# Performance work log

Hardware: AMD Instinct MI355X
Metric: run time of the kernel (lower is better)

## Reference

```python
import jax, jax.numpy as jnp
import numpy as np
from jax import lax

V, E, H, K = 100000, 256, 512, 12
B, T = 64, 256
START, END, PAD = 10, 11, 0
NEG = -100000.0


def setup_inputs() -> dict:
    key = jax.random.key(0)
    ks = jax.random.split(key, 16)
    Hd = H // 2
    def n(k, shape, s=0.1):
        return jax.random.normal(k, shape, jnp.float32) * s
    sentence = jax.random.randint(ks[0], (B, T), 0, V)
    sentence_chars = jnp.zeros((B, T, 16), jnp.int32)
    emb = jax.random.normal(ks[1], (V, E), jnp.float32)
    Wih_f, Whh_f = n(ks[2], (4 * Hd, E)), n(ks[3], (4 * Hd, Hd))
    bih_f, bhh_f = n(ks[4], (4 * Hd,)), n(ks[5], (4 * Hd,))
    Wih_b, Whh_b = n(ks[6], (4 * Hd, E)), n(ks[7], (4 * Hd, Hd))
    bih_b, bhh_b = n(ks[8], (4 * Hd,)), n(ks[9], (4 * Hd,))
    Wp, bp = n(ks[10], (K, H)), n(ks[11], (K,))
    # transitions[i, j] = score of transitioning from tag j to tag i
    trans = jax.random.normal(ks[12], (K, K), jnp.float32)
    trans = trans.at[START, :].set(NEG)
    trans = trans.at[:, END].set(NEG)
    trans = trans.at[:, PAD].set(NEG)
    trans = trans.at[PAD, :].set(NEG)
    trans = trans.at[PAD, PAD].set(0.0)
    trans = trans.at[PAD, END].set(0.0)
    h0 = jax.random.normal(ks[13], (2, B, Hd), jnp.float32)
    c0 = jax.random.normal(ks[14], (2, B, Hd), jnp.float32)
    return dict(sentence=sentence, sentence_chars=sentence_chars, emb=emb,
                Wih_f=Wih_f, Whh_f=Whh_f, bih_f=bih_f, bhh_f=bhh_f,
                Wih_b=Wih_b, Whh_b=Whh_b, bih_b=bih_b, bhh_b=bhh_b,
                Wp=Wp, bp=bp, transitions=trans, h0=h0, c0=c0)


def _lstm_dir(x, Wih, Whh, bih, bhh, h, c, reverse):
    # x: [B, T, E] -> hs: [B, T, Hd]; PyTorch LSTM gate order i,f,g,o
    def step(carry, xt):
        h, c = carry
        g = xt @ Wih.T + bih + h @ Whh.T + bhh
        i, f, gg, o = jnp.split(g, 4, axis=-1)
        c = jax.nn.sigmoid(f) * c + jax.nn.sigmoid(i) * jnp.tanh(gg)
        h = jax.nn.sigmoid(o) * jnp.tanh(c)
        return (h, c), h
    _, hs = lax.scan(step, (h, c), jnp.swapaxes(x, 0, 1), reverse=reverse)
    return jnp.swapaxes(hs, 0, 1)


def _viterbi(features, transitions, lengths):
    b, t, k = features.shape
    score0 = jnp.full((b, k), -10000.0, features.dtype).at[:, START].set(0.0)
    def step(score, feat_t):
        m = score[:, None, :] + transitions[None]  # [B, K(to), K(from)]
        bptr = jnp.argmax(m, axis=-1)              # [B, K]
        new = jnp.max(m, axis=-1) + feat_t
        return new, bptr
    final, bptrs = lax.scan(step, score0, jnp.swapaxes(features, 0, 1))  # bptrs [T,B,K]
    best_score = jnp.max(final, axis=-1)
    best_tag = jnp.argmax(final, axis=-1)
    ts = jnp.arange(t)
    def backtrack(x, inp):
        tt, bp = inp  # bp: [B, K]
        emit = x      # p_t (valid where tt < length)
        nxt = jnp.take_along_axis(bp, x[:, None], axis=1)[:, 0]
        x = jnp.where(tt < lengths, nxt, x)
        return x, emit
    _, ps = lax.scan(backtrack, best_tag, (ts, bptrs), reverse=True)  # [T, B]
    paths = jnp.swapaxes(ps, 0, 1)
    paths = jnp.where(jnp.arange(t)[None, :] < lengths[:, None], paths, -1)
    return paths, best_score


def reference(sentence, sentence_chars, emb, Wih_f, Whh_f, bih_f, bhh_f,
              Wih_b, Whh_b, bih_b, bhh_b, Wp, bp, transitions, h0, c0):
    mask = sentence > 0
    lengths = mask.sum(axis=1)
    x = emb[sentence]  # [B, T, E]
    hf = _lstm_dir(x, Wih_f, Whh_f, bih_f, bhh_f, h0[0], c0[0], False)
    hb = _lstm_dir(x, Wih_b, Whh_b, bih_b, bhh_b, h0[1], c0[1], True)
    feats = jnp.concatenate([hf, hb], axis=-1) @ Wp.T + bp  # [B, T, K]
    paths, best_score = _viterbi(feats, transitions, lengths)
    return paths, best_score
```

## Files before the change

### kernel.cpp

```cpp
#include <hip/hip_runtime.h>


#define NB 64
#define NT 256
#define NKTAG 12
#define START_TAG 10
#define KK_SLAB2 8
#define KK_REG2 56

typedef unsigned short u16;
typedef _Float16 half2v __attribute__((ext_vector_type(2)));
typedef _Float16 half8 __attribute__((ext_vector_type(8)));
typedef float f32x4 __attribute__((ext_vector_type(4)));

__device__ __forceinline__ float b2f(u16 u) {
  union { unsigned int i; float f; } v; v.i = ((unsigned int)u) << 16; return v.f;
}
__device__ __forceinline__ u16 f2b(float f) {
  union { float f; unsigned int i; } v; v.f = f;
  unsigned int r = v.i + 0x7FFFu + ((v.i >> 16) & 1u);
  return (u16)(r >> 16);
}
__device__ __forceinline__ u16 f2h(float f) {
  union { _Float16 h; u16 u; } v; v.h = (_Float16)f; return v.u;
}
__device__ __forceinline__ unsigned int pkh(float x, float y) {
  return (unsigned int)f2h(x) | ((unsigned int)f2h(y) << 16);
}
__device__ __forceinline__ float fsig(float x) { return 1.0f / (1.0f + __expf(-x)); }
__device__ __forceinline__ float ftanh(float x) { return 2.0f / (1.0f + __expf(-2.0f * x)) - 1.0f; }

__device__ __forceinline__ float dot2h(unsigned int a, unsigned int b, float c) {
#if __has_builtin(__builtin_amdgcn_fdot2)
  union { unsigned int u; half2v h; } va, vb;
  va.u = a; vb.u = b;
  return __builtin_amdgcn_fdot2(va.h, vb.h, c, false);
#else
  float d;
  asm("v_dot2_f32_f16 %0, %1, %2, %3" : "=v"(d) : "v"(a), "v"(b), "v"(c));
  return d;
#endif
}

__device__ __forceinline__ void barrier_lds() {
  asm volatile("s_waitcnt lgkmcnt(0)" ::: "memory");
  __builtin_amdgcn_s_barrier();
}

__global__ __launch_bounds__(256) void pack_whh(const float* __restrict__ Whf,
                                                const float* __restrict__ Whb,
                                                const float* __restrict__ Wp,
                                                uint4* __restrict__ WT,
                                                unsigned int* __restrict__ WpH) {
  if (blockIdx.x == 256) {
    for (int it = 0; it < 12; ++it) {
      int idx = it * 256 + threadIdx.x;
      int k = idx >> 8, cc = idx & 255;
      WpH[idx] = pkh(Wp[(size_t)k * 512 + 2 * cc], Wp[(size_t)k * 512 + 2 * cc + 1]);
    }
    return;
  }
  int gid = blockIdx.x * 256 + threadIdx.x;
  int d = gid >> 15;
  int rem = gid & 32767;
  int kk = rem >> 8, j = rem & 255;
  const float* W = d ? Whb : Whf;
  int k0 = kk * 2;
  uint4 o;
  o.x = pkh(W[(size_t)j * 256 + k0],         W[(size_t)j * 256 + k0 + 1]);
  o.y = pkh(W[(size_t)(j + 256) * 256 + k0], W[(size_t)(j + 256) * 256 + k0 + 1]);
  o.z = pkh(W[(size_t)(j + 512) * 256 + k0], W[(size_t)(j + 512) * 256 + k0 + 1]);
  o.w = pkh(W[(size_t)(j + 768) * 256 + k0], W[(size_t)(j + 768) * 256 + k0 + 1]);
  WT[gid] = o;
}

__global__ __launch_bounds__(256) void gemm_x(const int* __restrict__ sent,
                                              const float* __restrict__ emb,
                                              const float* __restrict__ Wf,
                                              const float* __restrict__ Wb,
                                              const float* __restrict__ bihf,
                                              const float* __restrict__ bhhf,
                                              const float* __restrict__ bihb,
                                              const float* __restrict__ bhhb,
                                              u16* __restrict__ X4) {
  __shared__ _Float16 A_lds[128][40];
  __shared__ _Float16 B_lds[64][40];
  __shared__ int tok[128];
  __shared__ u16 Xs[128][80];
  int tid = threadIdx.x;
  int lin = blockIdx.y * 32 + blockIdx.x;
  int swz = (lin & 7) * 512 + (lin >> 3);
  int in = swz & 31;
  int im = swz >> 5;
  int d = in >> 4, j0 = (in & 15) * 16;
  if (tid < 128) tok[tid] = sent[im * 128 + tid];

  int w = tid >> 6, l = tid & 63;
  int lrow = l & 15, lk = l >> 4;
  f32x4 acc[2][4];
#pragma unroll
  for (int mt = 0; mt < 2; ++mt)
#pragma unroll
    for (int nt = 0; nt < 4; ++nt) acc[mt][nt] = (f32x4)0.0f;

  int arow = tid >> 1, akh = tid & 1;
  int brow = tid & 63, bkq = tid >> 6;
  int r_w = ((brow >> 4) << 8) + j0 + (brow & 15);
  const float* wrow = (d ? Wb : Wf) + (size_t)r_w * 256;

  for (int kc = 0; kc < 8; ++kc) {
    int k0 = kc * 32;
    __syncthreads();
    {
      const float* ap = emb + (size_t)tok[arow] * 256 + k0 + akh * 16;
#pragma unroll
      for (int q = 0; q < 2; ++q) {
        float4 v0 = *(const float4*)(ap + q * 8);
        float4 v1 = *(const float4*)(ap + q * 8 + 4);
        uint4 pk;
        pk.x = pkh(v0.x, v0.y); pk.y = pkh(v0.z, v0.w);
        pk.z = pkh(v1.x, v1.y); pk.w = pkh(v1.z, v1.w);
        *(uint4*)&A_lds[arow][akh * 16 + q * 8] = pk;
      }
    }
    {
      float4 v0 = *(const float4*)(wrow + k0 + bkq * 8);
      float4 v1 = *(const float4*)(wrow + k0 + bkq * 8 + 4);
      uint4 pk;
      pk.x = pkh(v0.x, v0.y); pk.y = pkh(v0.z, v0.w);
      pk.z = pkh(v1.x, v1.y); pk.w = pkh(v1.z, v1.w);
      *(uint4*)&B_lds[brow][bkq * 8] = pk;
    }
    __syncthreads();
    half8 af[2], bf[4];
#pragma unroll
    for (int mt = 0; mt < 2; ++mt)
      af[mt] = *(const half8*)&A_lds[w * 32 + mt * 16 + lrow][lk * 8];
#pragma unroll
    for (int nt = 0; nt < 4; ++nt)
      bf[nt] = *(const half8*)&B_lds[nt * 16 + lrow][lk * 8];
#pragma unroll
    for (int mt = 0; mt < 2; ++mt)
#pragma unroll
      for (int nt = 0; nt < 4; ++nt)
        acc[mt][nt] = __builtin_amdgcn_mfma_f32_16x16x32_f16(af[mt], bf[nt], acc[mt][nt], 0, 0, 0);
  }
  float bias[4];
#pragma unroll
  for (int nt = 0; nt < 4; ++nt) {
    int rr = nt * 256 + j0 + lrow;
    bias[nt] = d ? (bihb[rr] + bhhb[rr]) : (bihf[rr] + bhhf[rr]);
  }
  __syncthreads();
#pragma unroll
  for (int mt = 0; mt < 2; ++mt)
#pragma unroll
    for (int r = 0; r < 4; ++r) {
      int row = w * 32 + mt * 16 + lk * 4 + r;
      uint2 pk;
      pk.x = (unsigned int)f2b(acc[mt][0][r] + bias[0]) |
             ((unsigned int)f2b(acc[mt][1][r] + bias[1]) << 16);
      pk.y = (unsigned int)f2b(acc[mt][2][r] + bias[2]) |
             ((unsigned int)f2b(acc[mt][3][r] + bias[3]) << 16);
      *(uint2*)&Xs[row][lrow * 4] = pk;
    }
  __syncthreads();
  int frow = tid >> 1, fh = tid & 1;
  int i = im * 128 + frow;
  int bb = i >> 8, tt = i & 255;
  size_t base = (((size_t)d * NT + tt) * NB + bb) * 1024 + (size_t)j0 * 4 + fh * 32;
#pragma unroll
  for (int q = 0; q < 4; ++q)
    *(uint4*)&X4[base + q * 8] = *(const uint4*)&Xs[frow][fh * 32 + q * 8];
}

__global__ __launch_bounds__(512, 2) void lstm_scan(const uint4* __restrict__ WT,
                                                    const ushort4* __restrict__ X4,
                                                    const float* __restrict__ h0,
                                                    const float* __restrict__ c0,
                                                    u16* __restrict__ H) {
  int d = blockIdx.x >> 6, b = blockIdx.x & 63;
  int tid = threadIdx.x;
  int jj = tid & 255, g = tid >> 8;
  __shared__ uint4 wlds[2 * KK_SLAB2 * 256];
  __shared__ uint4 h2s4[32];
  __shared__ float4 plds[256];
  const uint4* Ws = WT + (size_t)d * 32768;
  for (int e = tid; e < 2 * KK_SLAB2 * 256; e += 512) {
    int sr = e >> 8, j2 = e & 255;
    int gg = sr / KK_SLAB2, r = sr - gg * KK_SLAB2;
    wlds[e] = Ws[(size_t)(gg * 64 + r) * 256 + j2];
  }
  uint4 wreg[KK_REG2];
#pragma unroll
  for (int r = 0; r < KK_REG2; ++r)
    wreg[r] = Ws[(size_t)(g * 64 + KK_SLAB2 + r) * 256 + jj];
  float c = 0.f;
  if (g == 0) c = c0[((size_t)d * NB + b) * 256 + jj];
  if (tid < 256) ((u16*)h2s4)[tid] = f2h(h0[((size_t)d * NB + b) * 256 + tid]);
  __syncthreads();
  for (int s = 0; s < NT; ++s) {
    int t = d ? (NT - 1 - s) : s;
    ushort4 xg = make_ushort4(0, 0, 0, 0);
    if (g == 0) xg = X4[(((size_t)d * NT + t) * NB + b) * 256 + jj];
    float ai = 0.f, af = 0.f, ag = 0.f, ao = 0.f;
#pragma unroll
    for (int q = 0; q < 16; ++q) {
      uint4 h4 = h2s4[g * 16 + q];
      unsigned int hp[4] = {h4.x, h4.y, h4.z, h4.w};
#pragma unroll
      for (int e = 0; e < 4; ++e) {
        int kkl = q * 4 + e;
        uint4 wv;
        if (kkl < KK_SLAB2) wv = wlds[((g * KK_SLAB2 + kkl) << 8) | jj];
        else                wv = wreg[kkl - KK_SLAB2];
        ai = dot2h(wv.x, hp[e], ai); af = dot2h(wv.y, hp[e], af);
        ag = dot2h(wv.z, hp[e], ag); ao = dot2h(wv.w, hp[e], ao);
      }
    }
    if (g) plds[jj] = make_float4(ai, af, ag, ao);
    barrier_lds();
    if (g == 0) {
      float4 p0 = plds[jj];
      ai += p0.x + b2f(xg.x);
      af += p0.y + b2f(xg.y);
      ag += p0.z + b2f(xg.z);
      ao += p0.w + b2f(xg.w);
      float ii = fsig(ai), ff = fsig(af), gg2 = ftanh(ag), oo = fsig(ao);
      c = ff * c + ii * gg2;
      float h = oo * ftanh(c);
      u16 hu = f2h(h);
      ((u16*)h2s4)[jj] = hu;
      H[(((size_t)d * NB + b) * NT + t) * 256 + jj] = hu;
    }
    barrier_lds();
  }
}

__global__ __launch_bounds__(384) void feats_kernel(const u16* __restrict__ H,
                                                    const unsigned int* __restrict__ WpH,
                                                    const float* __restrict__ bp,
                                                    float* __restrict__ FT) {
  __shared__ uint4 hbuf[32][65];
  __shared__ uint4 wbuf[64][12];
  int tid = threadIdx.x;
  int i0 = blockIdx.x * 32;
  for (int idx = tid; idx < 768; idx += 384) {
    int it = idx / 12, k = idx - it * 12;
    wbuf[it][k] = ((const uint4*)WpH)[k * 64 + it];
  }
  for (int idx = tid; idx < 2048; idx += 384) {
    int row = idx >> 6, c4 = idx & 63;
    int i = i0 + row;
    int b = i >> 8, t = i & 255;
    int dd = c4 >> 5, cc = c4 & 31;
    const uint4* hpg = (const uint4*)(H + (((size_t)dd * NB + b) * NT + t) * 256);
    hbuf[row][c4] = hpg[cc];
  }
  __syncthreads();
  int row = tid / 12, k = tid - row * 12;
  float s0 = 0.f, s1 = 0.f, s2 = 0.f, s3 = 0.f;
#pragma unroll 8
  for (int it = 0; it < 64; ++it) {
    uint4 h4 = hbuf[row][it];
    uint4 w4 = wbuf[it][k];
    s0 = dot2h(h4.x, w4.x, s0); s1 = dot2h(h4.y, w4.y, s1);
    s2 = dot2h(h4.z, w4.z, s2); s3 = dot2h(h4.w, w4.w, s3);
  }
  int i = i0 + row;
  FT[(size_t)i * NKTAG + k] = (s0 + s1) + (s2 + s3) + bp[k];
}

__global__ __launch_bounds__(64) void viterbi_kernel(const float* __restrict__ FT,
                                                     const float* __restrict__ trans,
                                                     const int* __restrict__ sent,
                                                     float* __restrict__ out) {
  int b = blockIdx.x, tid = threadIdx.x;
  __shared__ float trans_s[12][12];
  __shared__ float s_s[12];
  __shared__ unsigned char bp_s[256][12];
  __shared__ int path_s[256];
  for (int idx = tid; idx < 144; idx += 64) trans_s[idx / 12][idx % 12] = trans[idx];
  int cnt = 0;
#pragma unroll
  for (int q = 0; q < 4; ++q) cnt += (sent[b * NT + q * 64 + tid] > 0) ? 1 : 0;
  for (int off = 32; off; off >>= 1) cnt += __shfl_down(cnt, off);
  int len = __shfl(cnt, 0);
  if (tid < 12) s_s[tid] = (tid == START_TAG) ? 0.f : -10000.f;
  float f_next = (tid < 12) ? FT[((size_t)b * NT) * NKTAG + tid] : 0.f;
  __syncthreads();
  for (int t = 0; t < NT; ++t) {
    float best = 0.f, f = f_next;
    int barg = 0;
    if (t + 1 < NT && tid < 12)
      f_next = FT[((size_t)b * NT + t + 1) * NKTAG + tid];
    if (tid < 12) {
      best = s_s[0] + trans_s[tid][0];
      barg = 0;
#pragma unroll
      for (int fr = 1; fr < 12; ++fr) {
        float v = s_s[fr] + trans_s[tid][fr];
        if (v > best) { best = v; barg = fr; }
      }
    }
    __syncthreads();
    if (tid < 12) {
      s_s[tid] = best + f;
      bp_s[t][tid] = (unsigned char)barg;
    }
    __syncthreads();
  }
  if (tid == 0) {
    float bs = s_s[0];
    int bt = 0;
    for (int k = 1; k < 12; ++k)
      if (s_s[k] > bs) { bs = s_s[k]; bt = k; }
    out[NB * NT + b] = bs;
    int x = bt;
    for (int tt = NT - 1; tt >= 0; --tt) {
      path_s[tt] = x;
      int nxt = bp_s[tt][x];
      if (tt < len) x = nxt;
    }
  }
  __syncthreads();
#pragma unroll
  for (int q = 0; q < 4; ++q) {
    int t = q * 64 + tid;
    out[b * NT + t] = (t < len) ? (float)path_s[t] : -1.0f;
  }
}

extern "C" void kernel_launch(void* const* d_in, const int* in_sizes, int n_in,
                              void* d_out, int out_size, void* d_ws, size_t ws_size,
                              hipStream_t stream) {
  (void)in_sizes; (void)n_in; (void)out_size; (void)ws_size;
  const int*   sent  = (const int*)d_in[0];
  const float* emb   = (const float*)d_in[2];
  const float* Wih_f = (const float*)d_in[3];
  const float* Whh_f = (const float*)d_in[4];
  const float* bih_f = (const float*)d_in[5];
  const float* bhh_f = (const float*)d_in[6];
  const float* Wih_b = (const float*)d_in[7];
  const float* Whh_b = (const float*)d_in[8];
  const float* bih_b = (const float*)d_in[9];
  const float* bhh_b = (const float*)d_in[10];
  const float* Wp    = (const float*)d_in[11];
  const float* bp    = (const float*)d_in[12];
  const float* trans = (const float*)d_in[13];
  const float* h0    = (const float*)d_in[14];
  const float* c0    = (const float*)d_in[15];
  float* out = (float*)d_out;

  char* w = (char*)d_ws;
  u16*   X4  = (u16*)w;
  uint4* WTH = (uint4*)(w + 67108864);
  float* FT  = (float*)(w + 68157440);
  unsigned int* WpH = (unsigned int*)(w + 68943872);
  u16*   H   = (u16*)(w + 68956160);

  pack_whh<<<dim3(257), dim3(256), 0, stream>>>(Whh_f, Whh_b, Wp, WTH, WpH);
  gemm_x<<<dim3(32, 128), dim3(256), 0, stream>>>(sent, emb, Wih_f, Wih_b,
                                                  bih_f, bhh_f, bih_b, bhh_b, X4);
  lstm_scan<<<dim3(128), dim3(512), 0, stream>>>(WTH, (const ushort4*)X4, h0, c0, H);
  feats_kernel<<<dim3(512), dim3(384), 0, stream>>>(H, WpH, bp, FT);
  viterbi_kernel<<<dim3(64), dim3(64), 0, stream>>>(FT, trans, sent, out);
}
```

Baseline: 559.0 us.

## Fuse weight packing into input GEMM and widen GEMM N-tile to 128

The separate pack_whh launch is folded into gemm_x as extra trailing blocks, which removes one kernel launch and its serialization. The GEMM tile is widened from 64 to 128 output columns per block (32 hidden units × 4 gates), halving the number of blocks and the redundant embedding gathers per column slice. The gather and fp16 conversion of A are now reused across twice as many MFMAs. In exchange, each block uses more registers and LDS, and there are fewer blocks to spread across the CUs.

```diff
diff --git a/kernel.cpp b/kernel.cpp
--- a/kernel.cpp
+++ b/kernel.cpp
@@ -47,65 +47,67 @@
   __builtin_amdgcn_s_barrier();
 }
 
-__global__ __launch_bounds__(256) void pack_whh(const float* __restrict__ Whf,
-                                                const float* __restrict__ Whb,
-                                                const float* __restrict__ Wp,
-                                                uint4* __restrict__ WT,
-                                                unsigned int* __restrict__ WpH) {
-  if (blockIdx.x == 256) {
-    for (int it = 0; it < 12; ++it) {
-      int idx = it * 256 + threadIdx.x;
-      int k = idx >> 8, cc = idx & 255;
-      WpH[idx] = pkh(Wp[(size_t)k * 512 + 2 * cc], Wp[(size_t)k * 512 + 2 * cc + 1]);
-    }
+__global__ __launch_bounds__(256, 2) void gemm_x(const int* __restrict__ sent,
+                                                 const float* __restrict__ emb,
+                                                 const float* __restrict__ Wf,
+                                                 const float* __restrict__ Wb,
+                                                 const float* __restrict__ bihf,
+                                                 const float* __restrict__ bhhf,
+                                                 const float* __restrict__ bihb,
+                                                 const float* __restrict__ bhhb,
+                                                 const float* __restrict__ Whf,
+                                                 const float* __restrict__ Whb,
+                                                 const float* __restrict__ Wp,
+                                                 uint4* __restrict__ WT,
+                                                 unsigned int* __restrict__ WpH,
+                                                 u16* __restrict__ X4) {
+  int tid = threadIdx.x;
+  if (blockIdx.x >= 2048) {
+    int pb = blockIdx.x - 2048;
+    if (pb == 256) {
+      for (int it = 0; it < 12; ++it) {
+        int idx = it * 256 + tid;
+        int k = idx >> 8, cc = idx & 255;
+        WpH[idx] = pkh(Wp[(size_t)k * 512 + 2 * cc], Wp[(size_t)k * 512 + 2 * cc + 1]);
+      }
+      return;
+    }
+    int gid = pb * 256 + tid;
+    int d = gid >> 15;
+    int rem = gid & 32767;
+    int kk = rem >> 8, j = rem & 255;
+    const float* W = d ? Whb : Whf;
+    int k0 = kk * 2;
+    uint4 o;
+    o.x = pkh(W[(size_t)j * 256 + k0],         W[(size_t)j * 256 + k0 + 1]);
+    o.y = pkh(W[(size_t)(j + 256) * 256 + k0], W[(size_t)(j + 256) * 256 + k0 + 1]);
+    o.z = pkh(W[(size_t)(j + 512) * 256 + k0], W[(size_t)(j + 512) * 256 + k0 + 1]);
+    o.w = pkh(W[(size_t)(j + 768) * 256 + k0], W[(size_t)(j + 768) * 256 + k0 + 1]);
+    WT[gid] = o;
     return;
   }
-  int gid = blockIdx.x * 256 + threadIdx.x;
-  int d = gid >> 15;
-  int rem = gid & 32767;
-  int kk = rem >> 8, j = rem & 255;
-  const float* W = d ? Whb : Whf;
-  int k0 = kk * 2;
-  uint4 o;
-  o.x = pkh(W[(size_t)j * 256 + k0],         W[(size_t)j * 256 + k0 + 1]);
-  o.y = pkh(W[(size_t)(j + 256) * 256 + k0], W[(size_t)(j + 256) * 256 + k0 + 1]);
-  o.z = pkh(W[(size_t)(j + 512) * 256 + k0], W[(size_t)(j + 512) * 256 + k0 + 1]);
-  o.w = pkh(W[(size_t)(j + 768) * 256 + k0], W[(size_t)(j + 768) * 256 + k0 + 1]);
-  WT[gid] = o;
-}
-
-__global__ __launch_bounds__(256) void gemm_x(const int* __restrict__ sent,
-                                              const float* __restrict__ emb,
-                                              const float* __restrict__ Wf,
-                                              const float* __restrict__ Wb,
-                                              const float* __restrict__ bihf,
-                                              const float* __restrict__ bhhf,
-                                              const float* __restrict__ bihb,
-                                              const float* __restrict__ bhhb,
-                                              u16* __restrict__ X4) {
   __shared__ _Float16 A_lds[128][40];
-  __shared__ _Float16 B_lds[64][40];
+  __shared__ _Float16 B_lds[128][40];
   __shared__ int tok[128];
-  __shared__ u16 Xs[128][80];
-  int tid = threadIdx.x;
-  int lin = blockIdx.y * 32 + blockIdx.x;
-  int swz = (lin & 7) * 512 + (lin >> 3);
-  int in = swz & 31;
-  int im = swz >> 5;
-  int d = in >> 4, j0 = (in & 15) * 16;
+  __shared__ u16 Xs[128][136];
+  int lin = blockIdx.x;
+  int swz = (lin & 7) * 256 + (lin >> 3);
+  int in = swz & 15;
+  int im = swz >> 4;
+  int d = in >> 3, j0 = (in & 7) * 32;
   if (tid < 128) tok[tid] = sent[im * 128 + tid];
 
   int w = tid >> 6, l = tid & 63;
   int lrow = l & 15, lk = l >> 4;
-  f32x4 acc[2][4];
+  f32x4 acc[2][8];
 #pragma unroll
   for (int mt = 0; mt < 2; ++mt)
 #pragma unroll
-    for (int nt = 0; nt < 4; ++nt) acc[mt][nt] = (f32x4)0.0f;
+    for (int nt = 0; nt < 8; ++nt) acc[mt][nt] = (f32x4)0.0f;
 
   int arow = tid >> 1, akh = tid & 1;
-  int brow = tid & 63, bkq = tid >> 6;
-  int r_w = ((brow >> 4) << 8) + j0 + (brow & 15);
+  int brow = tid & 127, bhalf = tid >> 7;
+  int r_w = ((brow >> 5) << 8) + j0 + (brow & 31);
   const float* wrow = (d ? Wb : Wf) + (size_t)r_w * 256;
 
   for (int kc = 0; kc < 8; ++kc) {
@@ -124,31 +126,36 @@
       }
     }
     {
-      float4 v0 = *(const float4*)(wrow + k0 + bkq * 8);
-      float4 v1 = *(const float4*)(wrow + k0 + bkq * 8 + 4);
-      uint4 pk;
-      pk.x = pkh(v0.x, v0.y); pk.y = pkh(v0.z, v0.w);
-      pk.z = pkh(v1.x, v1.y); pk.w = pkh(v1.z, v1.w);
-      *(uint4*)&B_lds[brow][bkq * 8] = pk;
+      const float* bp_ = wrow + k0 + bhalf * 16;
+#pragma unroll
+      for (int q = 0; q < 2; ++q) {
+        float4 v0 = *(const float4*)(bp_ + q * 8);
+        float4 v1 = *(const float4*)(bp_ + q * 8 + 4);
+        uint4 pk;
+        pk.x = pkh(v0.x, v0.y); pk.y = pkh(v0.z, v0.w);
+        pk.z = pkh(v1.x, v1.y); pk.w = pkh(v1.z, v1.w);
+        *(uint4*)&B_lds[brow][bhalf * 16 + q * 8] = pk;
+      }
     }
     __syncthreads();
-    half8 af[2], bf[4];
+    half8 af[2], bf[8];
 #pragma unroll
     for (int mt = 0; mt < 2; ++mt)
       af[mt] = *(const half8*)&A_lds[w * 32 + mt * 16 + lrow][lk * 8];
 #pragma unroll
-    for (int nt = 0; nt < 4; ++nt)
+    for (int nt = 0; nt < 8; ++nt)
       bf[nt] = *(const half8*)&B_lds[nt * 16 + lrow][lk * 8];
 #pragma unroll
     for (int mt = 0; mt < 2; ++mt)
 #pragma unroll
-      for (int nt = 0; nt < 4; ++nt)
+      for (int nt = 0; nt < 8; ++nt)
         acc[mt][nt] = __builtin_amdgcn_mfma_f32_16x16x32_f16(af[mt], bf[nt], acc[mt][nt], 0, 0, 0);
   }
-  float bias[4];
-#pragma unroll
-  for (int nt = 0; nt < 4; ++nt) {
-    int rr = nt * 256 + j0 + lrow;
+  float bias[8];
+#pragma unroll
+  for (int nt = 0; nt < 8; ++nt) {
+    int n = nt * 16 + lrow;
+    int rr = ((n >> 5) << 8) + j0 + (n & 31);
     bias[nt] = d ? (bihb[rr] + bhhb[rr]) : (bihf[rr] + bhhf[rr]);
   }
   __syncthreads();
@@ -157,21 +164,26 @@
 #pragma unroll
     for (int r = 0; r < 4; ++r) {
       int row = w * 32 + mt * 16 + lk * 4 + r;
-      uint2 pk;
-      pk.x = (unsigned int)f2b(acc[mt][0][r] + bias[0]) |
-             ((unsigned int)f2b(acc[mt][1][r] + bias[1]) << 16);
-      pk.y = (unsigned int)f2b(acc[mt][2][r] + bias[2]) |
+      uint2 p0, p1;
+      p0.x = (unsigned int)f2b(acc[mt][0][r] + bias[0]) |
+             ((unsigned int)f2b(acc[mt][2][r] + bias[2]) << 16);
+      p0.y = (unsigned int)f2b(acc[mt][4][r] + bias[4]) |
+             ((unsigned int)f2b(acc[mt][6][r] + bias[6]) << 16);
+      p1.x = (unsigned int)f2b(acc[mt][1][r] + bias[1]) |
              ((unsigned int)f2b(acc[mt][3][r] + bias[3]) << 16);
-      *(uint2*)&Xs[row][lrow * 4] = pk;
+      p1.y = (unsigned int)f2b(acc[mt][5][r] + bias[5]) |
+             ((unsigned int)f2b(acc[mt][7][r] + bias[7]) << 16);
+      *(uint2*)&Xs[row][lrow * 4] = p0;
+      *(uint2*)&Xs[row][(16 + lrow) * 4] = p1;
     }
   __syncthreads();
   int frow = tid >> 1, fh = tid & 1;
   int i = im * 128 + frow;
   int bb = i >> 8, tt = i & 255;
-  size_t base = (((size_t)d * NT + tt) * NB + bb) * 1024 + (size_t)j0 * 4 + fh * 32;
-#pragma unroll
-  for (int q = 0; q < 4; ++q)
-    *(uint4*)&X4[base + q * 8] = *(const uint4*)&Xs[frow][fh * 32 + q * 8];
+  size_t base = (((size_t)d * NT + tt) * NB + bb) * 1024 + (size_t)j0 * 4 + fh * 64;
+#pragma unroll
+  for (int q = 0; q < 8; ++q)
+    *(uint4*)&X4[base + q * 8] = *(const uint4*)&Xs[frow][fh * 64 + q * 8];
 }
 
 __global__ __launch_bounds__(512, 2) void lstm_scan(const uint4* __restrict__ WT,
@@ -359,9 +371,9 @@
   unsigned int* WpH = (unsigned int*)(w + 68943872);
   u16*   H   = (u16*)(w + 68956160);
 
-  pack_whh<<<dim3(257), dim3(256), 0, stream>>>(Whh_f, Whh_b, Wp, WTH, WpH);
-  gemm_x<<<dim3(32, 128), dim3(256), 0, stream>>>(sent, emb, Wih_f, Wih_b,
-                                                  bih_f, bhh_f, bih_b, bhh_b, X4);
+  gemm_x<<<dim3(2305), dim3(256), 0, stream>>>(sent, emb, Wih_f, Wih_b,
+                                               bih_f, bhh_f, bih_b, bhh_b,
+                                               Whh_f, Whh_b, Wp, WTH, WpH, X4);
   lstm_scan<<<dim3(128), dim3(512), 0, stream>>>(WTH, (const ushort4*)X4, h0, c0, H);
   feats_kernel<<<dim3(512), dim3(384), 0, stream>>>(H, WpH, bp, FT);
   viterbi_kernel<<<dim3(64), dim3(64), 0, stream>>>(FT, trans, sent, out);
```

New measurement: 550.4 us. About the same (-1.5%).
